# Kernel tuning notes

Hardware: AMD Instinct MI355X
Metric: run time of the kernel (lower is better)

Reference implementation:

```python
import jax, jax.numpy as jnp
import numpy as np

D = 1024          # d_input_feature
GCN_OUTS = [1024, 512, 256]
DEC_OUTS = [512, 1024, 1024]  # reversed[1:] + [d_input_feature]
EPS = 1e-3        # keras LayerNormalization default epsilon


def _ln(x, gamma, beta):
    m = jnp.mean(x, axis=-1, keepdims=True)
    v = jnp.mean(jnp.square(x - m), axis=-1, keepdims=True)
    return gamma * (x - m) * jax.lax.rsqrt(v + EPS) + beta


def _gcn(x, A, W, b, act):
    # message passing with dense adjacency: act((A @ x) @ W + b)
    h = jnp.einsum('bij,bjd->bid', A, x)
    return act(h @ W + b)


def setup_inputs() -> dict:
    key = jax.random.key(0)
    ks = jax.random.split(key, 40)
    B, DG, DC, NTT = 16384, 772, 100, 128
    inp = {
        't_1': jax.random.randint(ks[0], (B,), 0, NTT),
        'g_1': jax.random.normal(ks[1], (B, DG), jnp.float32),
        'c_1': jax.random.normal(ks[2], (B, DC), jnp.float32),
        'A_1': jax.random.uniform(ks[3], (B, 3, 3), jnp.float32),
        't_2': jax.random.randint(ks[4], (B,), 0, NTT),
        'g_2': jax.random.normal(ks[5], (B, DG), jnp.float32),
        'c_2': jax.random.normal(ks[6], (B, DC), jnp.float32),
        'A_2': jax.random.uniform(ks[7], (B, 3, 3), jnp.float32),
        'embed': jax.random.normal(ks[8], (NTT, D), jnp.float32) * 0.02,
        'Wt': jax.random.normal(ks[9], (D, D), jnp.float32) / np.sqrt(D),
        'bt': jnp.zeros((D,), jnp.float32),
        'Wg': jax.random.normal(ks[10], (DG, D), jnp.float32) / np.sqrt(DG),
        'bg': jnp.zeros((D,), jnp.float32),
        'Wc': jax.random.normal(ks[11], (DC, D), jnp.float32) / np.sqrt(DC),
        'bc': jnp.zeros((D,), jnp.float32),
        'ln_t_g': jnp.ones((D,), jnp.float32), 'ln_t_b': jnp.zeros((D,), jnp.float32),
        'ln_g_g': jnp.ones((D,), jnp.float32), 'ln_g_b': jnp.zeros((D,), jnp.float32),
        'ln_c_g': jnp.ones((D,), jnp.float32), 'ln_c_b': jnp.zeros((D,), jnp.float32),
    }
    d_in = D
    for i, d_out in enumerate(GCN_OUTS):
        inp[f'enc_W{i}'] = jax.random.normal(ks[12 + i], (d_in, d_out), jnp.float32) / np.sqrt(d_in)
        inp[f'enc_b{i}'] = jnp.zeros((d_out,), jnp.float32)
        d_in = d_out
    for i, d_out in enumerate(DEC_OUTS):
        inp[f'dec_W{i}'] = jax.random.normal(ks[20 + i], (d_in, d_out), jnp.float32) / np.sqrt(d_in)
        inp[f'dec_b{i}'] = jnp.zeros((d_out,), jnp.float32)
        d_in = d_out
    return inp


def _branch(t, g, c, embed, Wt, bt, Wg, bg, Wc, bc,
            ln_t_g, ln_t_b, ln_g_g, ln_g_b, ln_c_g, ln_c_b):
    te = embed[t]                               # [B, D]
    te = jax.nn.relu(te @ Wt + bt)
    ge = jax.nn.relu(g @ Wg + bg)
    ce = jax.nn.relu(c @ Wc + bc)
    te = _ln(te, ln_t_g, ln_t_b)
    ge = _ln(ge, ln_g_g, ln_g_b)
    ce = _ln(ce, ln_c_g, ln_c_b)
    return jnp.stack([te, ge, ce], axis=1)      # [B, 3, D]


def _encoder(X, A, enc):
    x = X
    for W, b in enc:
        x = _gcn(x, A, W, b, jax.nn.relu)
    return x


def _decoder(Z, A, dec):
    x = Z
    for W, b in dec:
        x = _gcn(x, A, W, b, jax.nn.silu)       # swish
    return x


def reference(t_1, g_1, c_1, A_1, t_2, g_2, c_2, A_2,
              embed, Wt, bt, Wg, bg, Wc, bc,
              ln_t_g, ln_t_b, ln_g_g, ln_g_b, ln_c_g, ln_c_b,
              enc_W0, enc_b0, enc_W1, enc_b1, enc_W2, enc_b2,
              dec_W0, dec_b0, dec_W1, dec_b1, dec_W2, dec_b2):
    enc = [(enc_W0, enc_b0), (enc_W1, enc_b1), (enc_W2, enc_b2)]
    dec = [(dec_W0, dec_b0), (dec_W1, dec_b1), (dec_W2, dec_b2)]
    bargs = (embed, Wt, bt, Wg, bg, Wc, bc,
             ln_t_g, ln_t_b, ln_g_g, ln_g_b, ln_c_g, ln_c_b)

    X_1 = _branch(t_1, g_1, c_1, *bargs)
    X_2 = _branch(t_2, g_2, c_2, *bargs)
    Z_1 = _encoder(X_1, A_1, enc)
    Z_2 = _encoder(X_2, A_2, enc)
    Z_loss = jnp.square(Z_1 - Z_2)              # [B, 3, 256]

    # GAE reconstruction path (recomputes X per the original code)
    X_h_1 = _decoder(Z_1, A_1, dec)
    X_h_2 = _decoder(Z_2, A_2, dec)
    X_loss = (jnp.square(X_1 - X_h_1) + jnp.square(X_2 - X_h_2)) / 2.0  # [B, 3, D]
    return Z_loss, X_loss
```

## Files before the change

kernel.cpp:

```cpp
#include <hip/hip_runtime.h>


typedef __attribute__((ext_vector_type(8))) short s16x8;
typedef __attribute__((ext_vector_type(4))) short s16x4;
typedef __attribute__((ext_vector_type(4))) float f32x4;

#define DEV static __device__ __forceinline__

DEV float b2f(ushort u) { return __builtin_bit_cast(float, (unsigned)u << 16); }
DEV ushort f2b(float f) {
  unsigned x = __builtin_bit_cast(unsigned, f);
  unsigned r = x + 0x7fffu + ((x >> 16) & 1u);
  return (ushort)(r >> 16);
}

typedef const __attribute__((address_space(1))) void* gas_ptr;
typedef __attribute__((address_space(3))) void* las_ptr;

template<int ACT>
__global__ __launch_bounds__(512, 2) void gemm256(
    const ushort* __restrict__ A, const ushort* __restrict__ BT,
    const float* __restrict__ bias, ushort* __restrict__ C,
    int M, int N, int K)
{
  __shared__ __align__(16) ushort ldsbuf[65536];
  char* Lb = (char*)ldsbuf;

  const int tid = threadIdx.x, lane = tid & 63, w = tid >> 6;
  const int wm = w >> 2, wn = w & 3;

  const int gx  = gridDim.x;
  const int nwg = gx * gridDim.y;
  const int wid = blockIdx.y * gx + blockIdx.x;
  const int q   = nwg >> 3;
  const int Lw  = (wid & 7) * q + (wid >> 3);
  const int bn  = Lw % gx;
  const int bm  = Lw / gx;

  const ushort* Abase = A  + (size_t)bm * 256 * K;
  const ushort* Bbase = BT + (size_t)bn * 256 * K;
  const int T = K >> 6;

  const int srow = w * 8 + (lane >> 3);
  const int scol = (((lane & 7) ^ (lane >> 3)) << 3);

#define STAGE(buf, m, half, Gb, k0)                                          \
  {                                                                          \
    _Pragma("unroll") for (int _j = 0; _j < 2; ++_j) {                       \
      const ushort* _src = (Gb) + (size_t)((half)*128 + _j*64 + srow) * K    \
                           + (k0) + scol;                                    \
      ushort* _dst = (ushort*)(Lb + ((buf)*2 + (m)) * 32768                  \
                               + ((half)*128 + _j*64 + w*8) * 128);          \
      __builtin_amdgcn_global_load_lds((gas_ptr)_src, (las_ptr)_dst, 16,0,0);\
    }                                                                        \
  }

  const int lr = lane & 15, lk = lane >> 4;

#define READ_A(dst, c, mh)                                                   \
  _Pragma("unroll") for (int _i = 0; _i < 4; ++_i)                           \
    _Pragma("unroll") for (int _kk = 0; _kk < 2; ++_kk) {                    \
      const int _r   = (mh)*128 + wm*64 + _i*16 + lr;                        \
      const int _cbb = _kk*64 + lk*16;                                       \
      dst[_i][_kk] = *(const s16x8*)(Lb + ((c)*2 + 0)*32768 + _r*128         \
                                     + (_cbb ^ ((_r & 7) << 4)));            \
    }
#define READ_B(dst, c, nh)                                                   \
  _Pragma("unroll") for (int _p = 0; _p < 2; ++_p)                           \
    _Pragma("unroll") for (int _kk = 0; _kk < 2; ++_kk) {                    \
      const int _r   = (nh)*128 + wn*32 + _p*16 + lr;                        \
      const int _cbb = _kk*64 + lk*16;                                       \
      dst[_p][_kk] = *(const s16x8*)(Lb + ((c)*2 + 1)*32768 + _r*128         \
                                     + (_cbb ^ ((_r & 7) << 4)));            \
    }

#define MFMA_Q(mh, nh)                                                       \
  _Pragma("unroll") for (int _i = 0; _i < 4; ++_i)                           \
    _Pragma("unroll") for (int _p = 0; _p < 2; ++_p)                         \
      _Pragma("unroll") for (int _kk = 0; _kk < 2; ++_kk)                    \
        acc[(mh)*4 + _i][(nh)*2 + _p] =                                      \
            __builtin_amdgcn_mfma_f32_16x16x32_bf16(                         \
                af[_i][_kk], bf[_p][_kk], acc[(mh)*4 + _i][(nh)*2 + _p],     \
                0, 0, 0);

#define MIDBAR  do { __builtin_amdgcn_s_barrier();                           \
                     asm volatile("s_waitcnt lgkmcnt(0)" ::: "memory");      \
                     __builtin_amdgcn_sched_barrier(0);                      \
                     __builtin_amdgcn_s_setprio(1); } while (0)
#define ENDBAR  do { __builtin_amdgcn_s_setprio(0);                          \
                     __builtin_amdgcn_s_barrier(); } while (0)

  f32x4 acc[8][4];
  #pragma unroll
  for (int i = 0; i < 8; ++i)
    #pragma unroll
    for (int j = 0; j < 4; ++j) acc[i][j] = f32x4{0.f, 0.f, 0.f, 0.f};

  STAGE(0, 0, 0, Abase, 0);
  STAGE(0, 1, 0, Bbase, 0);
  STAGE(0, 1, 1, Bbase, 0);
  STAGE(0, 0, 1, Abase, 0);
  STAGE(1, 0, 0, Abase, 64);
  STAGE(1, 1, 1, Bbase, 64);
  STAGE(1, 0, 1, Abase, 64);
  asm volatile("s_waitcnt vmcnt(6)" ::: "memory");
  __builtin_amdgcn_s_barrier();

  for (int t = 0; t < T; ++t) {
    const int cbuf = t & 1, nbuf = cbuf ^ 1;
    const int k1 = ((t + 1 < T) ? t + 1 : t + 1 - T) * 64;
    const int k2 = ((t + 2 < T) ? t + 2 : t + 2 - T) * 64;
    s16x8 af[4][2], bf[2][2];
    READ_A(af, cbuf, 0);
    READ_B(bf, cbuf, 0);
    STAGE(nbuf, 1, 0, Bbase, k1);
    asm volatile("s_waitcnt lgkmcnt(8)" ::: "memory");
    MIDBAR; MFMA_Q(0, 0); ENDBAR;
    READ_B(bf, cbuf, 1);
    STAGE(cbuf, 0, 0, Abase, k2);
    MIDBAR; MFMA_Q(0, 1); ENDBAR;
    READ_A(af, cbuf, 1);
    STAGE(cbuf, 1, 1, Bbase, k2);
    MIDBAR; MFMA_Q(1, 1); ENDBAR;
    READ_B(bf, cbuf, 0);
    STAGE(cbuf, 0, 1, Abase, k2);
    MIDBAR; MFMA_Q(1, 0);
    __builtin_amdgcn_s_setprio(0);
    asm volatile("s_waitcnt vmcnt(6)" ::: "memory");
    __builtin_amdgcn_s_barrier();
  }

  const int row0 = bm * 256, col0 = bn * 256;
  #pragma unroll
  for (int mi = 0; mi < 8; ++mi) {
    const int row = row0 + (mi >> 2) * 128 + wm * 64 + (mi & 3) * 16 + lk * 4;
    #pragma unroll
    for (int ni = 0; ni < 4; ++ni) {
      const int col = col0 + (ni >> 1) * 128 + wn * 32 + (ni & 1) * 16 + lr;
      const float bv = bias[col];
      #pragma unroll
      for (int r = 0; r < 4; ++r) {
        float v = acc[mi][ni][r] + bv;
        if (ACT == 0) v = fmaxf(v, 0.f);
        else          v = v / (1.f + __expf(-v));
        C[(size_t)(row + r) * N + col] = f2b(v);
      }
    }
  }
#undef STAGE
#undef READ_A
#undef READ_B
#undef MFMA_Q
#undef MIDBAR
#undef ENDBAR
}

template<int ACT>
__global__ __launch_bounds__(256) void gemm_bt(
    const ushort* __restrict__ A, const ushort* __restrict__ BT,
    const float* __restrict__ bias, ushort* __restrict__ C,
    int M, int N, int K)
{
  __shared__ ushort As[128 * 64];
  __shared__ ushort Bs[128 * 64];

  const int tid  = threadIdx.x;
  const int lane = tid & 63;
  const int w    = tid >> 6;

  const int gx  = gridDim.x;
  const int nwg = gx * gridDim.y;
  const int wid = blockIdx.y * gx + blockIdx.x;
  const int q   = nwg >> 3;
  const int L   = (wid & 7) * q + (wid >> 3);
  const int bn  = L % gx;
  const int bm  = L / gx;

  const int wm = w >> 1, wn = w & 1;
  const int lr = lane & 15;
  const int lk = lane >> 4;

  const ushort* Abase = A  + (size_t)bm * 128 * K;
  const ushort* Bbase = BT + (size_t)bn * 128 * K;
  const int srow = w * 8 + (lane >> 3);
  const int scol = (lane & 7) * 8;

  f32x4 acc[4][4];
  #pragma unroll
  for (int i = 0; i < 4; i++)
    #pragma unroll
    for (int j = 0; j < 4; j++) acc[i][j] = f32x4{0.f, 0.f, 0.f, 0.f};

  for (int k0 = 0; k0 < K; k0 += 64) {
    #pragma unroll
    for (int i = 0; i < 4; i++) {
      const int r = srow + i * 32;
      __builtin_amdgcn_global_load_lds(
          (gas_ptr)(Abase + (size_t)r * K + k0 + scol),
          (las_ptr)(As + w * 512 + i * 2048), 16, 0, 0);
    }
    #pragma unroll
    for (int i = 0; i < 4; i++) {
      const int r = srow + i * 32;
      __builtin_amdgcn_global_load_lds(
          (gas_ptr)(Bbase + (size_t)r * K + k0 + scol),
          (las_ptr)(Bs + w * 512 + i * 2048), 16, 0, 0);
    }
    __syncthreads();

    #pragma unroll
    for (int kc = 0; kc < 64; kc += 32) {
      s16x8 af[4], bf[4];
      #pragma unroll
      for (int mi = 0; mi < 4; mi++)
        af[mi] = *(const s16x8*)&As[(wm * 64 + mi * 16 + lr) * 64 + kc + lk * 8];
      #pragma unroll
      for (int ni = 0; ni < 4; ni++)
        bf[ni] = *(const s16x8*)&Bs[(wn * 64 + ni * 16 + lr) * 64 + kc + lk * 8];
      #pragma unroll
      for (int mi = 0; mi < 4; mi++)
        #pragma unroll
        for (int ni = 0; ni < 4; ni++)
          acc[mi][ni] = __builtin_amdgcn_mfma_f32_16x16x32_bf16(
              af[mi], bf[ni], acc[mi][ni], 0, 0, 0);
    }
    __syncthreads();
  }

  const int row0 = bm * 128 + wm * 64;
  const int col0 = bn * 128 + wn * 64;
  #pragma unroll
  for (int ni = 0; ni < 4; ni++) {
    const int col = col0 + ni * 16 + lr;
    const float bv = bias[col];
    #pragma unroll
    for (int mi = 0; mi < 4; mi++) {
      const int row = row0 + mi * 16 + lk * 4;
      #pragma unroll
      for (int r = 0; r < 4; r++) {
        float v = acc[mi][ni][r] + bv;
        if (ACT == 0) v = fmaxf(v, 0.f);
        else          v = v / (1.f + __expf(-v));
        C[(size_t)(row + r) * N + col] = f2b(v);
      }
    }
  }
}

__global__ void trans_conv(const float* __restrict__ W, ushort* __restrict__ WT,
                           int K, int N, int Kpad)
{
  __shared__ float tile[32][33];
  const int n0 = blockIdx.x * 32, k0 = blockIdx.y * 32;
  const int tx = threadIdx.x, ty = threadIdx.y;
  #pragma unroll
  for (int r = 0; r < 4; r++) {
    const int k = k0 + ty + r * 8;
    tile[ty + r * 8][tx] = (k < K) ? W[(size_t)k * N + n0 + tx] : 0.f;
  }
  __syncthreads();
  #pragma unroll
  for (int r = 0; r < 4; r++) {
    const int n = n0 + ty + r * 8;
    WT[(size_t)n * Kpad + k0 + tx] = f2b(tile[tx][ty + r * 8]);
  }
}

__global__ void conv_pad(const float* __restrict__ in, ushort* __restrict__ out,
                         int R, int Cin, int Cpad)
{
  const int gid = blockIdx.x * 256 + threadIdx.x;
  if (gid >= R * Cpad) return;
  const int r = gid / Cpad, c = gid - r * Cpad;
  out[gid] = (c < Cin) ? f2b(in[(size_t)r * Cin + c]) : (ushort)0;
}

DEV void ln_row(const ushort* __restrict__ in, const float* __restrict__ gamma,
                const float* __restrict__ beta, ushort* __restrict__ outp,
                int tid, float* red)
{
  s16x4 v = *(const s16x4*)&in[tid * 4];
  const float x0 = b2f((ushort)v[0]), x1 = b2f((ushort)v[1]);
  const float x2 = b2f((ushort)v[2]), x3 = b2f((ushort)v[3]);
  float s = x0 + x1 + x2 + x3;
  float qq = x0 * x0 + x1 * x1 + x2 * x2 + x3 * x3;
  #pragma unroll
  for (int o = 32; o > 0; o >>= 1) { s += __shfl_down(s, o); qq += __shfl_down(qq, o); }
  const int wv = tid >> 6, lane = tid & 63;
  __syncthreads();
  if (lane == 0) { red[wv] = s; red[4 + wv] = qq; }
  __syncthreads();
  s  = red[0] + red[1] + red[2] + red[3];
  qq = red[4] + red[5] + red[6] + red[7];
  const float m   = s * (1.f / 1024.f);
  const float var = qq * (1.f / 1024.f) - m * m;
  const float rs  = rsqrtf(var + 1e-3f);
  const int c = tid * 4;
  s16x4 o;
  o[0] = (short)f2b(gamma[c + 0] * ((x0 - m) * rs) + beta[c + 0]);
  o[1] = (short)f2b(gamma[c + 1] * ((x1 - m) * rs) + beta[c + 1]);
  o[2] = (short)f2b(gamma[c + 2] * ((x2 - m) * rs) + beta[c + 2]);
  o[3] = (short)f2b(gamma[c + 3] * ((x3 - m) * rs) + beta[c + 3]);
  *(s16x4*)&outp[c] = o;
}

__global__ void ln_te(const ushort* __restrict__ in, const float* __restrict__ g,
                      const float* __restrict__ b, ushort* __restrict__ out)
{
  __shared__ float red[8];
  ln_row(in + (size_t)blockIdx.x * 1024, g, b,
         out + (size_t)blockIdx.x * 1024, threadIdx.x, red);
}

__global__ void assembleX(const int* __restrict__ t, const ushort* __restrict__ tetab,
                          const ushort* __restrict__ ge, const ushort* __restrict__ ce,
                          const float* __restrict__ gG, const float* __restrict__ gB,
                          const float* __restrict__ cG, const float* __restrict__ cB,
                          ushort* __restrict__ X)
{
  __shared__ float red[8];
  const int b = blockIdx.x, tid = threadIdx.x;
  const int tt = t[b];
  *(s16x4*)&X[(size_t)b * 3072 + tid * 4] =
      *(const s16x4*)&tetab[(size_t)tt * 1024 + tid * 4];
  ln_row(ge + (size_t)b * 1024, gG, gB, X + (size_t)b * 3072 + 1024, tid, red);
  ln_row(ce + (size_t)b * 1024, cG, cB, X + (size_t)b * 3072 + 2048, tid, red);
}

__global__ void mix3(const ushort* __restrict__ x, const float* __restrict__ Am,
                     ushort* __restrict__ out, int d, int lg, int nB)
{
  const int gid = blockIdx.x * 256 + threadIdx.x;
  const int b = gid >> lg;
  if (b >= nB) return;
  const int c8 = (gid & ((1 << lg) - 1)) << 3;
  const ushort* xb = x   + (size_t)b * 3 * d + c8;
  ushort*       ob = out + (size_t)b * 3 * d + c8;
  s16x8 x0 = *(const s16x8*)xb;
  s16x8 x1 = *(const s16x8*)(xb + d);
  s16x8 x2 = *(const s16x8*)(xb + 2 * d);
  float f0[8], f1[8], f2[8];
  #pragma unroll
  for (int e = 0; e < 8; e++) {
    f0[e] = b2f((ushort)x0[e]); f1[e] = b2f((ushort)x1[e]); f2[e] = b2f((ushort)x2[e]);
  }
  const float* Ab = Am + (size_t)b * 9;
  #pragma unroll
  for (int j = 0; j < 3; j++) {
    const float a0 = Ab[j * 3], a1 = Ab[j * 3 + 1], a2 = Ab[j * 3 + 2];
    s16x8 o;
    #pragma unroll
    for (int e = 0; e < 8; e++)
      o[e] = (short)f2b(a0 * f0[e] + a1 * f1[e] + a2 * f2[e]);
    *(s16x8*)(ob + j * d) = o;
  }
}

__global__ void zloss_k(const ushort* __restrict__ z1, const ushort* __restrict__ z2,
                        float* __restrict__ out, int n8)
{
  const int gid = blockIdx.x * 256 + threadIdx.x;
  if (gid >= n8) return;
  const size_t i = (size_t)gid * 8;
  s16x8 a = *(const s16x8*)&z1[i];
  s16x8 b = *(const s16x8*)&z2[i];
  f32x4 o0, o1;
  #pragma unroll
  for (int e = 0; e < 4; e++) {
    float d0 = b2f((ushort)a[e]) - b2f((ushort)b[e]);
    float d1 = b2f((ushort)a[e + 4]) - b2f((ushort)b[e + 4]);
    o0[e] = d0 * d0; o1[e] = d1 * d1;
  }
  *(f32x4*)&out[i] = o0; *(f32x4*)&out[i + 4] = o1;
}

template<int ADD>
__global__ void xloss_k(const ushort* __restrict__ X, const ushort* __restrict__ Xh,
                        float* __restrict__ out, int n8)
{
  const int gid = blockIdx.x * 256 + threadIdx.x;
  if (gid >= n8) return;
  const size_t i = (size_t)gid * 8;
  s16x8 a = *(const s16x8*)&X[i];
  s16x8 b = *(const s16x8*)&Xh[i];
  f32x4 o0, o1;
  #pragma unroll
  for (int e = 0; e < 4; e++) {
    float d0 = b2f((ushort)a[e]) - b2f((ushort)b[e]);
    float d1 = b2f((ushort)a[e + 4]) - b2f((ushort)b[e + 4]);
    o0[e] = 0.5f * d0 * d0; o1[e] = 0.5f * d1 * d1;
  }
  if (ADD) {
    f32x4 p0 = *(const f32x4*)&out[i];
    f32x4 p1 = *(const f32x4*)&out[i + 4];
    #pragma unroll
    for (int e = 0; e < 4; e++) { o0[e] += p0[e]; o1[e] += p1[e]; }
  }
  *(f32x4*)&out[i] = o0; *(f32x4*)&out[i + 4] = o1;
}

extern "C" void kernel_launch(void* const* d_in, const int* in_sizes, int n_in,
                              void* d_out, int out_size, void* d_ws, size_t ws_size,
                              hipStream_t stream)
{
  const int B = 16384, S = 3 * B;
  const int*   t1 = (const int*)d_in[0];
  const float* g1 = (const float*)d_in[1];
  const float* c1 = (const float*)d_in[2];
  const float* A1 = (const float*)d_in[3];
  const int*   t2 = (const int*)d_in[4];
  const float* g2 = (const float*)d_in[5];
  const float* c2 = (const float*)d_in[6];
  const float* A2 = (const float*)d_in[7];
  const float* embed = (const float*)d_in[8];
  const float* Wt = (const float*)d_in[9];  const float* bt = (const float*)d_in[10];
  const float* Wg = (const float*)d_in[11]; const float* bg = (const float*)d_in[12];
  const float* Wc = (const float*)d_in[13]; const float* bc = (const float*)d_in[14];
  const float* lntg = (const float*)d_in[15]; const float* lntb = (const float*)d_in[16];
  const float* lngg = (const float*)d_in[17]; const float* lngb = (const float*)d_in[18];
  const float* lncg = (const float*)d_in[19]; const float* lncb = (const float*)d_in[20];
  const float* eW0 = (const float*)d_in[21]; const float* eb0 = (const float*)d_in[22];
  const float* eW1 = (const float*)d_in[23]; const float* eb1 = (const float*)d_in[24];
  const float* eW2 = (const float*)d_in[25]; const float* eb2 = (const float*)d_in[26];
  const float* dW0 = (const float*)d_in[27]; const float* db0 = (const float*)d_in[28];
  const float* dW1 = (const float*)d_in[29]; const float* db1 = (const float*)d_in[30];
  const float* dW2 = (const float*)d_in[31]; const float* db2 = (const float*)d_in[32];
  float* out = (float*)d_out;
  (void)in_sizes; (void)n_in; (void)out_size; (void)ws_size;

  char* ws = (char*)d_ws; size_t off = 0;
  auto alloc = [&](size_t bytes) -> void* {
    void* p = ws + off; off += (bytes + 255) & ~(size_t)255; return p;
  };
  ushort* WtT  = (ushort*)alloc((size_t)1024 * 1024 * 2);
  ushort* WgT  = (ushort*)alloc((size_t)1024 * 896 * 2);
  ushort* WcT  = (ushort*)alloc((size_t)1024 * 128 * 2);
  ushort* E0T  = (ushort*)alloc((size_t)1024 * 1024 * 2);
  ushort* E1T  = (ushort*)alloc((size_t)512 * 1024 * 2);
  ushort* E2T  = (ushort*)alloc((size_t)256 * 512 * 2);
  ushort* D0T  = (ushort*)alloc((size_t)512 * 256 * 2);
  ushort* D1T  = (ushort*)alloc((size_t)1024 * 512 * 2);
  ushort* D2T  = (ushort*)alloc((size_t)1024 * 1024 * 2);
  ushort* embB = (ushort*)alloc((size_t)128 * 1024 * 2);
  ushort* teraw= (ushort*)alloc((size_t)128 * 1024 * 2);
  ushort* tetab= (ushort*)alloc((size_t)128 * 1024 * 2);
  ushort* gB[2] = {(ushort*)alloc((size_t)B * 896 * 2), (ushort*)alloc((size_t)B * 896 * 2)};
  ushort* cB[2] = {(ushort*)alloc((size_t)B * 128 * 2), (ushort*)alloc((size_t)B * 128 * 2)};
  ushort* zB[2] = {(ushort*)alloc((size_t)S * 256 * 2), (ushort*)alloc((size_t)S * 256 * 2)};
  ushort* Xb = (ushort*)alloc((size_t)S * 1024 * 2);
  ushort* b0 = (ushort*)alloc((size_t)S * 1024 * 2);
  ushort* b1 = (ushort*)alloc((size_t)S * 1024 * 2);

  const dim3 TB(32, 8);
  trans_conv<<<dim3(32, 32), TB, 0, stream>>>(Wt,  WtT, 1024, 1024, 1024);
  trans_conv<<<dim3(32, 28), TB, 0, stream>>>(Wg,  WgT,  772, 1024,  896);
  trans_conv<<<dim3(32,  4), TB, 0, stream>>>(Wc,  WcT,  100, 1024,  128);
  trans_conv<<<dim3(32, 32), TB, 0, stream>>>(eW0, E0T, 1024, 1024, 1024);
  trans_conv<<<dim3(16, 32), TB, 0, stream>>>(eW1, E1T, 1024,  512, 1024);
  trans_conv<<<dim3( 8, 16), TB, 0, stream>>>(eW2, E2T,  512,  256,  512);
  trans_conv<<<dim3(16,  8), TB, 0, stream>>>(dW0, D0T,  256,  512,  256);
  trans_conv<<<dim3(32, 16), TB, 0, stream>>>(dW1, D1T,  512, 1024,  512);
  trans_conv<<<dim3(32, 32), TB, 0, stream>>>(dW2, D2T, 1024, 1024, 1024);
  conv_pad<<<512, 256, 0, stream>>>(embed, embB, 128, 1024, 1024);
  conv_pad<<<(B * 896 + 255) / 256, 256, 0, stream>>>(g1, gB[0], B, 772, 896);
  conv_pad<<<(B * 896 + 255) / 256, 256, 0, stream>>>(g2, gB[1], B, 772, 896);
  conv_pad<<<B * 128 / 256, 256, 0, stream>>>(c1, cB[0], B, 100, 128);
  conv_pad<<<B * 128 / 256, 256, 0, stream>>>(c2, cB[1], B, 100, 128);
  gemm_bt<0><<<dim3(8, 1), 256, 0, stream>>>(embB, WtT, bt, teraw, 128, 1024, 1024);
  ln_te<<<128, 256, 0, stream>>>(teraw, lntg, lntb, tetab);

  const size_t ZLEN = (size_t)S * 256;
  for (int br = 0; br < 2; ++br) {
    const int*   t    = br ? t2 : t1;
    const float* Aadj = br ? A2 : A1;
    gemm256<0><<<dim3(4, B / 256), 512, 0, stream>>>(gB[br], WgT, bg, b0, B, 1024, 896);
    gemm256<0><<<dim3(4, B / 256), 512, 0, stream>>>(cB[br], WcT, bc, b1, B, 1024, 128);
    assembleX<<<B, 256, 0, stream>>>(t, tetab, b0, b1, lngg, lngb, lncg, lncb, Xb);
    mix3<<<(B << 7) / 256, 256, 0, stream>>>(Xb, Aadj, b0, 1024, 7, B);
    gemm256<0><<<dim3(4, S / 256), 512, 0, stream>>>(b0, E0T, eb0, b1, S, 1024, 1024);
    mix3<<<(B << 7) / 256, 256, 0, stream>>>(b1, Aadj, b0, 1024, 7, B);
    gemm256<0><<<dim3(2, S / 256), 512, 0, stream>>>(b0, E1T, eb1, b1, S, 512, 1024);
    mix3<<<(B << 6) / 256, 256, 0, stream>>>(b1, Aadj, b0, 512, 6, B);
    gemm256<0><<<dim3(1, S / 256), 512, 0, stream>>>(b0, E2T, eb2, zB[br], S, 256, 512);
    mix3<<<(B << 5) / 256, 256, 0, stream>>>(zB[br], Aadj, b0, 256, 5, B);
    gemm256<1><<<dim3(2, S / 256), 512, 0, stream>>>(b0, D0T, db0, b1, S, 512, 256);
    mix3<<<(B << 6) / 256, 256, 0, stream>>>(b1, Aadj, b0, 512, 6, B);
    gemm256<1><<<dim3(4, S / 256), 512, 0, stream>>>(b0, D1T, db1, b1, S, 1024, 512);
    mix3<<<(B << 7) / 256, 256, 0, stream>>>(b1, Aadj, b0, 1024, 7, B);
    gemm256<1><<<dim3(4, S / 256), 512, 0, stream>>>(b0, D2T, db2, b1, S, 1024, 1024);
    if (br == 0)
      xloss_k<0><<<S * 1024 / 8 / 256, 256, 0, stream>>>(Xb, b1, out + ZLEN, S * 1024 / 8);
    else
      xloss_k<1><<<S * 1024 / 8 / 256, 256, 0, stream>>>(Xb, b1, out + ZLEN, S * 1024 / 8);
  }
  zloss_k<<<S * 256 / 8 / 256, 256, 0, stream>>>(zB[0], zB[1], out, S * 256 / 8);
}
```

Baseline: 1.572 ms.

## Add double-buffered swizzled 128-tile GEMM for small GEMMs and fuse X-loss

Turns the simple 128x128 GEMM into a double-buffered kernel with XOR-swizzled LDS. It replaces the 256-tile GEMM with it for the small-K or narrow-N layers (c projection, enc layer 2, dec layer 0), which gives those launches more workgroups to fill the device. It also keeps X and Xh from branch 1 in extra workspace so one kernel computes the averaged X loss, instead of a write pass followed by a read-modify-write pass. This needs more workspace, and falls back to the old path when the workspace is too small.

```diff
diff --git a/kernel.cpp b/kernel.cpp
--- a/kernel.cpp
+++ b/kernel.cpp
@@ -156,95 +156,108 @@
 }
 
 template<int ACT>
-__global__ __launch_bounds__(256) void gemm_bt(
+__global__ __launch_bounds__(256, 2) void gemm128(
     const ushort* __restrict__ A, const ushort* __restrict__ BT,
     const float* __restrict__ bias, ushort* __restrict__ C,
     int M, int N, int K)
 {
-  __shared__ ushort As[128 * 64];
-  __shared__ ushort Bs[128 * 64];
-
-  const int tid  = threadIdx.x;
-  const int lane = tid & 63;
-  const int w    = tid >> 6;
+  __shared__ __align__(16) ushort lds[32768];
+  char* Lb = (char*)lds;
+
+  const int tid = threadIdx.x, lane = tid & 63;
+  const int w = tid >> 6;
+  const int wm = w >> 1, wn = w & 1;
 
   const int gx  = gridDim.x;
   const int nwg = gx * gridDim.y;
   const int wid = blockIdx.y * gx + blockIdx.x;
   const int q   = nwg >> 3;
-  const int L   = (wid & 7) * q + (wid >> 3);
-  const int bn  = L % gx;
-  const int bm  = L / gx;
-
-  const int wm = w >> 1, wn = w & 1;
-  const int lr = lane & 15;
-  const int lk = lane >> 4;
+  const int Lw  = (wid & 7) * q + (wid >> 3);
+  const int bn  = Lw % gx;
+  const int bm  = Lw / gx;
 
   const ushort* Abase = A  + (size_t)bm * 128 * K;
   const ushort* Bbase = BT + (size_t)bn * 128 * K;
-  const int srow = w * 8 + (lane >> 3);
-  const int scol = (lane & 7) * 8;
+  const int T = K >> 6;
+
+  const int srow = tid >> 3;
+  const int scol = (((tid & 7) ^ (srow & 7)) << 3);
+
+#define STAGE128(buf, k0)                                                    \
+  {                                                                          \
+    _Pragma("unroll") for (int _j = 0; _j < 4; ++_j)                         \
+      __builtin_amdgcn_global_load_lds(                                      \
+          (gas_ptr)(Abase + (size_t)(_j * 32 + srow) * K + (k0) + scol),     \
+          (las_ptr)(Lb + (buf) + _j * 4096 + tid * 16), 16, 0, 0);           \
+    _Pragma("unroll") for (int _j = 0; _j < 4; ++_j)                         \
+      __builtin_amdgcn_global_load_lds(                                      \
+          (gas_ptr)(Bbase + (size_t)(_j * 32 + srow) * K + (k0) + scol),     \
+          (las_ptr)(Lb + (buf) + 16384 + _j * 4096 + tid * 16), 16, 0, 0);   \
+  }
+
+  const int lr = lane & 15, lk = lane >> 4;
 
   f32x4 acc[4][4];
   #pragma unroll
-  for (int i = 0; i < 4; i++)
-    #pragma unroll
-    for (int j = 0; j < 4; j++) acc[i][j] = f32x4{0.f, 0.f, 0.f, 0.f};
-
-  for (int k0 = 0; k0 < K; k0 += 64) {
-    #pragma unroll
-    for (int i = 0; i < 4; i++) {
-      const int r = srow + i * 32;
-      __builtin_amdgcn_global_load_lds(
-          (gas_ptr)(Abase + (size_t)r * K + k0 + scol),
-          (las_ptr)(As + w * 512 + i * 2048), 16, 0, 0);
-    }
-    #pragma unroll
-    for (int i = 0; i < 4; i++) {
-      const int r = srow + i * 32;
-      __builtin_amdgcn_global_load_lds(
-          (gas_ptr)(Bbase + (size_t)r * K + k0 + scol),
-          (las_ptr)(Bs + w * 512 + i * 2048), 16, 0, 0);
-    }
-    __syncthreads();
-
-    #pragma unroll
-    for (int kc = 0; kc < 64; kc += 32) {
-      s16x8 af[4], bf[4];
+  for (int f = 0; f < 4; ++f)
+    #pragma unroll
+    for (int p = 0; p < 4; ++p) acc[f][p] = f32x4{0.f, 0.f, 0.f, 0.f};
+
+  STAGE128(0, 0);
+  __syncthreads();
+
+  for (int t = 0; t < T; ++t) {
+    const int cb = (t & 1) << 15, nb = cb ^ 32768;
+    if (t + 1 < T) STAGE128(nb, (t + 1) << 6);
+
+    s16x8 af[4][2], bf[4][2];
+    #pragma unroll
+    for (int f = 0; f < 4; ++f)
       #pragma unroll
-      for (int mi = 0; mi < 4; mi++)
-        af[mi] = *(const s16x8*)&As[(wm * 64 + mi * 16 + lr) * 64 + kc + lk * 8];
+      for (int kk = 0; kk < 2; ++kk) {
+        const int r = wm * 64 + f * 16 + lr;
+        af[f][kk] = *(const s16x8*)(Lb + cb + r * 128
+                                    + ((kk * 64 + lk * 16) ^ ((r & 7) << 4)));
+      }
+    #pragma unroll
+    for (int p = 0; p < 4; ++p)
       #pragma unroll
-      for (int ni = 0; ni < 4; ni++)
-        bf[ni] = *(const s16x8*)&Bs[(wn * 64 + ni * 16 + lr) * 64 + kc + lk * 8];
+      for (int kk = 0; kk < 2; ++kk) {
+        const int r = wn * 64 + p * 16 + lr;
+        bf[p][kk] = *(const s16x8*)(Lb + cb + 16384 + r * 128
+                                    + ((kk * 64 + lk * 16) ^ ((r & 7) << 4)));
+      }
+    #pragma unroll
+    for (int f = 0; f < 4; ++f)
       #pragma unroll
-      for (int mi = 0; mi < 4; mi++)
+      for (int p = 0; p < 4; ++p)
         #pragma unroll
-        for (int ni = 0; ni < 4; ni++)
-          acc[mi][ni] = __builtin_amdgcn_mfma_f32_16x16x32_bf16(
-              af[mi], bf[ni], acc[mi][ni], 0, 0, 0);
-    }
+        for (int kk = 0; kk < 2; ++kk)
+          acc[f][p] = __builtin_amdgcn_mfma_f32_16x16x32_bf16(
+              af[f][kk], bf[p][kk], acc[f][p], 0, 0, 0);
+
     __syncthreads();
   }
 
   const int row0 = bm * 128 + wm * 64;
   const int col0 = bn * 128 + wn * 64;
   #pragma unroll
-  for (int ni = 0; ni < 4; ni++) {
-    const int col = col0 + ni * 16 + lr;
-    const float bv = bias[col];
-    #pragma unroll
-    for (int mi = 0; mi < 4; mi++) {
-      const int row = row0 + mi * 16 + lk * 4;
+  for (int f = 0; f < 4; ++f) {
+    const int row = row0 + f * 16 + lk * 4;
+    #pragma unroll
+    for (int p = 0; p < 4; ++p) {
+      const int col = col0 + p * 16 + lr;
+      const float bv = bias[col];
       #pragma unroll
-      for (int r = 0; r < 4; r++) {
-        float v = acc[mi][ni][r] + bv;
+      for (int r = 0; r < 4; ++r) {
+        float v = acc[f][p][r] + bv;
         if (ACT == 0) v = fmaxf(v, 0.f);
         else          v = v / (1.f + __expf(-v));
         C[(size_t)(row + r) * N + col] = f2b(v);
       }
     }
   }
+#undef STAGE128
 }
 
 __global__ void trans_conv(const float* __restrict__ W, ushort* __restrict__ WT,
@@ -370,6 +383,30 @@
     float d0 = b2f((ushort)a[e]) - b2f((ushort)b[e]);
     float d1 = b2f((ushort)a[e + 4]) - b2f((ushort)b[e + 4]);
     o0[e] = d0 * d0; o1[e] = d1 * d1;
+  }
+  *(f32x4*)&out[i] = o0; *(f32x4*)&out[i + 4] = o1;
+}
+
+__global__ void xloss2_k(const ushort* __restrict__ X1, const ushort* __restrict__ Xh1,
+                         const ushort* __restrict__ X2, const ushort* __restrict__ Xh2,
+                         float* __restrict__ out, int n8)
+{
+  const int gid = blockIdx.x * 256 + threadIdx.x;
+  if (gid >= n8) return;
+  const size_t i = (size_t)gid * 8;
+  s16x8 a1 = *(const s16x8*)&X1[i];
+  s16x8 h1 = *(const s16x8*)&Xh1[i];
+  s16x8 a2 = *(const s16x8*)&X2[i];
+  s16x8 h2 = *(const s16x8*)&Xh2[i];
+  f32x4 o0, o1;
+  #pragma unroll
+  for (int e = 0; e < 4; e++) {
+    float d1a = b2f((ushort)a1[e])     - b2f((ushort)h1[e]);
+    float d2a = b2f((ushort)a2[e])     - b2f((ushort)h2[e]);
+    float d1b = b2f((ushort)a1[e + 4]) - b2f((ushort)h1[e + 4]);
+    float d2b = b2f((ushort)a2[e + 4]) - b2f((ushort)h2[e + 4]);
+    o0[e] = 0.5f * (d1a * d1a + d2a * d2a);
+    o1[e] = 0.5f * (d1b * d1b + d2b * d2b);
   }
   *(f32x4*)&out[i] = o0; *(f32x4*)&out[i + 4] = o1;
 }
@@ -426,7 +463,7 @@
   const float* dW1 = (const float*)d_in[29]; const float* db1 = (const float*)d_in[30];
   const float* dW2 = (const float*)d_in[31]; const float* db2 = (const float*)d_in[32];
   float* out = (float*)d_out;
-  (void)in_sizes; (void)n_in; (void)out_size; (void)ws_size;
+  (void)in_sizes; (void)n_in; (void)out_size;
 
   char* ws = (char*)d_ws; size_t off = 0;
   auto alloc = [&](size_t bytes) -> void* {
@@ -447,9 +484,12 @@
   ushort* gB[2] = {(ushort*)alloc((size_t)B * 896 * 2), (ushort*)alloc((size_t)B * 896 * 2)};
   ushort* cB[2] = {(ushort*)alloc((size_t)B * 128 * 2), (ushort*)alloc((size_t)B * 128 * 2)};
   ushort* zB[2] = {(ushort*)alloc((size_t)S * 256 * 2), (ushort*)alloc((size_t)S * 256 * 2)};
-  ushort* Xb = (ushort*)alloc((size_t)S * 1024 * 2);
-  ushort* b0 = (ushort*)alloc((size_t)S * 1024 * 2);
-  ushort* b1 = (ushort*)alloc((size_t)S * 1024 * 2);
+  ushort* Xb0 = (ushort*)alloc((size_t)S * 1024 * 2);
+  ushort* b0  = (ushort*)alloc((size_t)S * 1024 * 2);
+  ushort* b1  = (ushort*)alloc((size_t)S * 1024 * 2);
+  ushort* Xb1 = (ushort*)alloc((size_t)S * 1024 * 2);
+  ushort* xh1 = (ushort*)alloc((size_t)S * 1024 * 2);
+  const bool fused = (off <= ws_size);
 
   const dim3 TB(32, 8);
   trans_conv<<<dim3(32, 32), TB, 0, stream>>>(Wt,  WtT, 1024, 1024, 1024);
@@ -466,32 +506,41 @@
   conv_pad<<<(B * 896 + 255) / 256, 256, 0, stream>>>(g2, gB[1], B, 772, 896);
   conv_pad<<<B * 128 / 256, 256, 0, stream>>>(c1, cB[0], B, 100, 128);
   conv_pad<<<B * 128 / 256, 256, 0, stream>>>(c2, cB[1], B, 100, 128);
-  gemm_bt<0><<<dim3(8, 1), 256, 0, stream>>>(embB, WtT, bt, teraw, 128, 1024, 1024);
+  gemm128<0><<<dim3(8, 1), 256, 0, stream>>>(embB, WtT, bt, teraw, 128, 1024, 1024);
   ln_te<<<128, 256, 0, stream>>>(teraw, lntg, lntb, tetab);
 
   const size_t ZLEN = (size_t)S * 256;
+  const int n8x = S * 1024 / 8;
   for (int br = 0; br < 2; ++br) {
     const int*   t    = br ? t2 : t1;
     const float* Aadj = br ? A2 : A1;
+    ushort* Xb = (fused && br) ? Xb1 : Xb0;
     gemm256<0><<<dim3(4, B / 256), 512, 0, stream>>>(gB[br], WgT, bg, b0, B, 1024, 896);
-    gemm256<0><<<dim3(4, B / 256), 512, 0, stream>>>(cB[br], WcT, bc, b1, B, 1024, 128);
+    gemm128<0><<<dim3(8, B / 128), 256, 0, stream>>>(cB[br], WcT, bc, b1, B, 1024, 128);
     assembleX<<<B, 256, 0, stream>>>(t, tetab, b0, b1, lngg, lngb, lncg, lncb, Xb);
     mix3<<<(B << 7) / 256, 256, 0, stream>>>(Xb, Aadj, b0, 1024, 7, B);
     gemm256<0><<<dim3(4, S / 256), 512, 0, stream>>>(b0, E0T, eb0, b1, S, 1024, 1024);
     mix3<<<(B << 7) / 256, 256, 0, stream>>>(b1, Aadj, b0, 1024, 7, B);
     gemm256<0><<<dim3(2, S / 256), 512, 0, stream>>>(b0, E1T, eb1, b1, S, 512, 1024);
     mix3<<<(B << 6) / 256, 256, 0, stream>>>(b1, Aadj, b0, 512, 6, B);
-    gemm256<0><<<dim3(1, S / 256), 512, 0, stream>>>(b0, E2T, eb2, zB[br], S, 256, 512);
+    gemm128<0><<<dim3(2, S / 128), 256, 0, stream>>>(b0, E2T, eb2, zB[br], S, 256, 512);
     mix3<<<(B << 5) / 256, 256, 0, stream>>>(zB[br], Aadj, b0, 256, 5, B);
-    gemm256<1><<<dim3(2, S / 256), 512, 0, stream>>>(b0, D0T, db0, b1, S, 512, 256);
+    gemm128<1><<<dim3(4, S / 128), 256, 0, stream>>>(b0, D0T, db0, b1, S, 512, 256);
     mix3<<<(B << 6) / 256, 256, 0, stream>>>(b1, Aadj, b0, 512, 6, B);
     gemm256<1><<<dim3(4, S / 256), 512, 0, stream>>>(b0, D1T, db1, b1, S, 1024, 512);
     mix3<<<(B << 7) / 256, 256, 0, stream>>>(b1, Aadj, b0, 1024, 7, B);
-    gemm256<1><<<dim3(4, S / 256), 512, 0, stream>>>(b0, D2T, db2, b1, S, 1024, 1024);
-    if (br == 0)
-      xloss_k<0><<<S * 1024 / 8 / 256, 256, 0, stream>>>(Xb, b1, out + ZLEN, S * 1024 / 8);
-    else
-      xloss_k<1><<<S * 1024 / 8 / 256, 256, 0, stream>>>(Xb, b1, out + ZLEN, S * 1024 / 8);
+    if (fused) {
+      ushort* xh = br ? b1 : xh1;
+      gemm256<1><<<dim3(4, S / 256), 512, 0, stream>>>(b0, D2T, db2, xh, S, 1024, 1024);
+      if (br)
+        xloss2_k<<<n8x / 256, 256, 0, stream>>>(Xb0, xh1, Xb1, b1, out + ZLEN, n8x);
+    } else {
+      gemm256<1><<<dim3(4, S / 256), 512, 0, stream>>>(b0, D2T, db2, b1, S, 1024, 1024);
+      if (br == 0)
+        xloss_k<0><<<n8x / 256, 256, 0, stream>>>(Xb0, b1, out + ZLEN, n8x);
+      else
+        xloss_k<1><<<n8x / 256, 256, 0, stream>>>(Xb0, b1, out + ZLEN, n8x);
+    }
   }
   zloss_k<<<S * 256 / 8 / 256, 256, 0, stream>>>(zB[0], zB[1], out, S * 256 / 8);
 }
```

New measurement: 1.506 ms. 4.2% less time.
